# Kernel optimization log

Measured on AMD Instinct MI355X. Metric: run time of the kernel, lower is better.

## Reference

```python
import jax, jax.numpy as jnp
import numpy as np
from jax import lax

PAD = 960          # tf.pad amount each side
LN_EPS = 1e-3      # keras LayerNormalization default epsilon


def _process(x, h, gamma, beta):
    """SmallConvNet: grouped 1D conv (per-channel learnable kernel) -> LayerNorm -> SiLU.
    x: (B, 2, 64), h: (2, 961) -> (B, 2, 1024). Dropout omitted (see notes)."""
    # grouped conv: each of the 2 'sequence' channels has its own length-961 kernel
    y = lax.conv_general_dilated(
        x, h[:, None, :],                 # kernel (O=2, I=1, W=961)
        window_strides=(1,), padding=[(PAD, PAD)],
        dimension_numbers=("NCH", "OIH", "NCH"),
        feature_group_count=2)            # (B, 2, 1024)
    mu = jnp.mean(y, axis=-1, keepdims=True)
    var = jnp.mean(jnp.square(y - mu), axis=-1, keepdims=True)
    ln = gamma * (y - mu) * lax.rsqrt(var + LN_EPS) + beta
    return jax.nn.silu(ln)


def reference(values, h, gamma, beta, symbols):
    # values: (B, 2, 64); symbols: (2, 64)
    vp = _process(values, h, gamma, beta)                              # (B, 2, 1024)
    sp = _process(jnp.zeros_like(values) + symbols, h, gamma, beta)    # (B, 2, 1024)
    # sign-based cosine-similarity attention: S[b,i,j] = mean_d sign(vp[b,j,d])*sign(vp[b,j,d]+sp[b,i,d])
    Xi = vp[:, None, :, :]   # (B, 1, N, D)
    Xj = sp[:, :, None, :]   # (B, N, 1, D)
    S = jnp.mean(jnp.sign(Xi) * jnp.sign(Xi + Xj), axis=-1)           # (B, N, N)
    scores = jax.nn.softmax(S, axis=-1)
    attn = jnp.einsum("bij,bjd->bid", scores, vp)                     # (B, N, D)
    return jax.nn.silu(attn * sp)


def setup_inputs() -> dict:
    key = jax.random.key(0)
    k1, k2, k3 = jax.random.split(key, 3)
    B, N, Din, D = 16384, 2, 64, 1024
    return {
        "values": jax.random.normal(k1, (B, N, Din), dtype=jnp.float32),
        "h": jax.random.normal(k2, (2, 961), dtype=jnp.float32),
        "gamma": jnp.ones((D,), dtype=jnp.float32),
        "beta": jnp.zeros((D,), dtype=jnp.float32),
        "symbols": jax.random.normal(k3, (N, Din), dtype=jnp.float32),
    }
```

## Files before the change

kernel.cpp:

```cpp
#include <hip/hip_runtime.h>

#define NB 4
#define LN_EPS 1e-3f

static __device__ __forceinline__ float sgnf(float x) {
    return (x > 0.f) ? 1.f : ((x < 0.f) ? -1.f : 0.f);
}
static __device__ __forceinline__ float siluf(float x) {
    return x / (1.f + __expf(-x));
}


__global__ __launch_bounds__(256) void hd_prep(
    const float* __restrict__ h, const float* __restrict__ symbols,
    const float* __restrict__ gamma, const float* __restrict__ beta,
    float* __restrict__ ws)
{
    __shared__ float h_pad[2][1088];
    __shared__ float x_s[2][64];
    __shared__ float red[4][2];
    const int t = threadIdx.x;

    for (int idx = t; idx < 2 * 1088; idx += 256) {
        const int c = idx / 1088, j = idx - c * 1088;
        float v = 0.f;
        if (j >= 63 && j <= 1023) v = h[c * 961 + (j - 63)];
        h_pad[c][j] = v;
        const int src = 1086 - j;
        float vr = 0.f;
        if (src >= 63 && src <= 1023) vr = h[c * 961 + (src - 63)];
        ws[c * 1088 + j] = vr;
    }
    if (t < 128) x_s[t >> 6][t & 63] = symbols[t];
    __syncthreads();

    const int c = t >> 7, tt = t & 127;
    const int lane = t & 63, wid = t >> 6;
    const int jbase = 1023 - tt;

    float acc[8];
    #pragma unroll
    for (int k = 0; k < 8; ++k) acc[k] = 0.f;

    #pragma unroll 8
    for (int i = 0; i < 64; ++i) {
        const float xv = x_s[c][i];
        #pragma unroll
        for (int k = 0; k < 8; ++k)
            acc[k] = fmaf(xv, h_pad[c][jbase + i - 128 * k], acc[k]);
    }

    float ps = 0.f, pq = 0.f;
    #pragma unroll
    for (int k = 0; k < 8; ++k) { ps += acc[k]; pq += acc[k] * acc[k]; }
    #pragma unroll
    for (int off = 32; off; off >>= 1) {
        ps += __shfl_xor(ps, off);
        pq += __shfl_xor(pq, off);
    }
    if (lane == 0) { red[wid][0] = ps; red[wid][1] = pq; }
    __syncthreads();

    const float sum = red[2 * c][0] + red[2 * c + 1][0];
    const float sq  = red[2 * c][1] + red[2 * c + 1][1];
    const float mu  = sum * (1.f / 1024.f);
    float var = sq * (1.f / 1024.f) - mu * mu;
    var = fmaxf(var, 0.f);
    const float rs = rsqrtf(var + LN_EPS);

    #pragma unroll
    for (int k = 0; k < 8; ++k) {
        const int d = tt + 128 * k;
        const float ln = (acc[k] - mu) * rs * gamma[d] + beta[d];
        ws[2176 + c * 1024 + d] = siluf(ln);
    }
}

__global__ __launch_bounds__(256, 4) void hd_main(
    const float* __restrict__ values,
    const float* __restrict__ gamma, const float* __restrict__ beta,
    const float* __restrict__ ws, float* __restrict__ out)
{
    __shared__ float hrev[2][1088];
    __shared__ float red[4][16];
    __shared__ float redf[16];
    __shared__ float red2[4][16];
    __shared__ float redf2[16];

    const int t = threadIdx.x;
    const int lane = t & 63, wid = t >> 6;
    const size_t b0 = (size_t)blockIdx.x * NB;

    for (int idx = t; idx < 2 * 1088; idx += 256)
        (&hrev[0][0])[idx] = ws[idx];
    __syncthreads();

    float acc[NB][2][4];
    #pragma unroll
    for (int b = 0; b < NB; ++b)
        #pragma unroll
        for (int c = 0; c < 2; ++c)
            #pragma unroll
            for (int k = 0; k < 4; ++k) acc[b][c][k] = 0.f;

    #pragma unroll 1
    for (int i0 = 0; i0 < 64; i0 += 8) {
        const int q0 = 56 + 4 * t - i0;
        float r[2][12];
        #pragma unroll
        for (int c = 0; c < 2; ++c) {
            const float4* p = reinterpret_cast<const float4*>(&hrev[c][q0]);
            const float4 a0 = p[0], a1 = p[1], a2 = p[2];
            r[c][0] = a0.x; r[c][1] = a0.y; r[c][2]  = a0.z; r[c][3]  = a0.w;
            r[c][4] = a1.x; r[c][5] = a1.y; r[c][6]  = a1.z; r[c][7]  = a1.w;
            r[c][8] = a2.x; r[c][9] = a2.y; r[c][10] = a2.z; r[c][11] = a2.w;
        }
        #pragma unroll
        for (int b = 0; b < NB; ++b) {
            #pragma unroll
            for (int c = 0; c < 2; ++c) {
                const float* xp = values + ((b0 + b) * 2 + c) * 64 + i0;
                #pragma unroll
                for (int il = 0; il < 8; ++il) {
                    const float xv = xp[il];
                    #pragma unroll
                    for (int k = 0; k < 4; ++k)
                        acc[b][c][k] = fmaf(xv, r[c][7 - il + k], acc[b][c][k]);
                }
            }
        }
    }

    {
        float v16[16];
        #pragma unroll
        for (int b = 0; b < NB; ++b)
            #pragma unroll
            for (int c = 0; c < 2; ++c) {
                const float a0 = acc[b][c][0], a1 = acc[b][c][1];
                const float a2 = acc[b][c][2], a3 = acc[b][c][3];
                v16[(b * 2 + c) * 2]     = a0 + a1 + a2 + a3;
                v16[(b * 2 + c) * 2 + 1] = a0 * a0 + a1 * a1 + a2 * a2 + a3 * a3;
            }
        #pragma unroll
        for (int off = 32; off; off >>= 1)
            #pragma unroll
            for (int v = 0; v < 16; ++v)
                v16[v] += __shfl_xor(v16[v], off);
        if (lane == 0) {
            #pragma unroll
            for (int v = 0; v < 16; ++v) red[wid][v] = v16[v];
        }
    }
    __syncthreads();
    if (t < 16) redf[t] = red[0][t] + red[1][t] + red[2][t] + red[3][t];
    __syncthreads();

    const float4 g4  = *reinterpret_cast<const float4*>(&gamma[4 * t]);
    const float4 be4 = *reinterpret_cast<const float4*>(&beta[4 * t]);
    float sp_r[2][4];
    #pragma unroll
    for (int a = 0; a < 2; ++a) {
        const float4 s4 = *reinterpret_cast<const float4*>(&ws[2176 + a * 1024 + 4 * t]);
        sp_r[a][0] = s4.x; sp_r[a][1] = s4.y; sp_r[a][2] = s4.z; sp_r[a][3] = s4.w;
    }
    const float gk[4] = {g4.x, g4.y, g4.z, g4.w};
    const float bk[4] = {be4.x, be4.y, be4.z, be4.w};

    #pragma unroll
    for (int b = 0; b < NB; ++b)
        #pragma unroll
        for (int c = 0; c < 2; ++c) {
            const float sum = redf[(b * 2 + c) * 2];
            const float sq  = redf[(b * 2 + c) * 2 + 1];
            const float mu  = sum * (1.f / 1024.f);
            float var = sq * (1.f / 1024.f) - mu * mu;
            var = fmaxf(var, 0.f);
            const float rs = rsqrtf(var + LN_EPS);
            #pragma unroll
            for (int k = 0; k < 4; ++k)
                acc[b][c][k] = siluf((acc[b][c][k] - mu) * rs * gk[k] + bk[k]);
        }

    {
        float v16[16];
        #pragma unroll
        for (int b = 0; b < NB; ++b)
            #pragma unroll
            for (int a = 0; a < 2; ++a)
                #pragma unroll
                for (int c = 0; c < 2; ++c) {
                    float s = 0.f;
                    #pragma unroll
                    for (int k = 0; k < 4; ++k)
                        s += sgnf(acc[b][c][k]) * sgnf(acc[b][c][k] + sp_r[a][k]);
                    v16[b * 4 + a * 2 + c] = s;
                }
        #pragma unroll
        for (int off = 32; off; off >>= 1)
            #pragma unroll
            for (int v = 0; v < 16; ++v)
                v16[v] += __shfl_xor(v16[v], off);
        if (lane == 0) {
            #pragma unroll
            for (int v = 0; v < 16; ++v) red2[wid][v] = v16[v];
        }
    }
    __syncthreads();
    if (t < 16) redf2[t] = red2[0][t] + red2[1][t] + red2[2][t] + red2[3][t];
    __syncthreads();

    #pragma unroll
    for (int b = 0; b < NB; ++b) {
        #pragma unroll
        for (int a = 0; a < 2; ++a) {
            const float s0 = redf2[b * 4 + a * 2 + 0] * (1.f / 1024.f);
            const float s1 = redf2[b * 4 + a * 2 + 1] * (1.f / 1024.f);
            const float m  = fmaxf(s0, s1);
            const float e0 = __expf(s0 - m), e1 = __expf(s1 - m);
            const float inv = 1.f / (e0 + e1);
            const float p0 = e0 * inv, p1 = e1 * inv;
            float4 o;
            o.x = siluf((p0 * acc[b][0][0] + p1 * acc[b][1][0]) * sp_r[a][0]);
            o.y = siluf((p0 * acc[b][0][1] + p1 * acc[b][1][1]) * sp_r[a][1]);
            o.z = siluf((p0 * acc[b][0][2] + p1 * acc[b][1][2]) * sp_r[a][2]);
            o.w = siluf((p0 * acc[b][0][3] + p1 * acc[b][1][3]) * sp_r[a][3]);
            *reinterpret_cast<float4*>(out + ((b0 + b) * 2 + a) * 1024 + 4 * t) = o;
        }
    }
}

extern "C" void kernel_launch(void* const* d_in, const int* in_sizes, int n_in,
                              void* d_out, int out_size, void* d_ws, size_t ws_size,
                              hipStream_t stream) {
    const float* values  = (const float*)d_in[0];
    const float* h       = (const float*)d_in[1];
    const float* gamma   = (const float*)d_in[2];
    const float* beta    = (const float*)d_in[3];
    const float* symbols = (const float*)d_in[4];
    float* out = (float*)d_out;
    float* ws  = (float*)d_ws;

    const int B = in_sizes[0] / 128;

    hipLaunchKernelGGL(hd_prep, dim3(1), dim3(256), 0, stream,
                       h, symbols, gamma, beta, ws);
    hipLaunchKernelGGL(hd_main, dim3(B / NB), dim3(256), 0, stream,
                       values, gamma, beta, ws, out);
}
```

Measured before the change: 131.3 us.

## Compute grouped conv with bf16x3 split MFMA using a prepacked Toeplitz B matrix

Recasts the per-channel 961-tap convolution as a matrix multiply on MFMA units. Each fp32 operand is split into three bf16 parts and recombined with eight 16x16x32 MFMAs to keep close to fp32 accuracy. A new prep kernel packs the Toeplitz filter matrix into MFMA lane layout in the workspace. The sign-product reduction is also replaced by integer sign-bit XOR counting. The path needs a larger workspace, falling back to the scalar kernel otherwise, and it adds an extra launch and per-tile B loads from global memory.

```diff
diff --git a/kernel.cpp b/kernel.cpp
--- a/kernel.cpp
+++ b/kernel.cpp
@@ -1,17 +1,333 @@
 #include <hip/hip_runtime.h>
 
-#define NB 4
 #define LN_EPS 1e-3f
+
+typedef __attribute__((ext_vector_type(8))) short bf16x8;
+typedef __attribute__((ext_vector_type(4))) float f32x4;
 
 static __device__ __forceinline__ float sgnf(float x) {
     return (x > 0.f) ? 1.f : ((x < 0.f) ? -1.f : 0.f);
 }
-static __device__ __forceinline__ float siluf(float x) {
-    return x / (1.f + __expf(-x));
-}
-
-
-__global__ __launch_bounds__(256) void hd_prep(
+static __device__ __forceinline__ float siluf(float x) { return x / (1.f + __expf(-x)); }
+
+static __device__ __forceinline__ unsigned short f2bf(float f) {
+    unsigned int u = __float_as_uint(f);
+    return (unsigned short)((u + 0x7fffu + ((u >> 16) & 1u)) >> 16);
+}
+static __device__ __forceinline__ float bf2f(unsigned short s) {
+    return __uint_as_float(((unsigned int)s) << 16);
+}
+static __device__ __forceinline__ void split3(float v, unsigned short& hi,
+                                              unsigned short& mid, unsigned short& lo) {
+    hi = f2bf(v);
+    const float r1 = v - bf2f(hi);
+    mid = f2bf(r1);
+    const float r2 = r1 - bf2f(mid);
+    lo = f2bf(r2);
+}
+
+#define SPOFF 196608
+
+__global__ __launch_bounds__(256) void hd_prep_sp(
+    const float* __restrict__ h, const float* __restrict__ symbols,
+    const float* __restrict__ gamma, const float* __restrict__ beta,
+    float* __restrict__ ws)
+{
+    __shared__ float h_pad[2][1088];
+    __shared__ float x_s[2][64];
+    __shared__ float red[4][2];
+    const int t = threadIdx.x;
+
+    for (int idx = t; idx < 2 * 1088; idx += 256) {
+        const int c = idx / 1088, j = idx - c * 1088;
+        float v = 0.f;
+        if (j >= 63 && j <= 1023) v = h[c * 961 + (j - 63)];
+        h_pad[c][j] = v;
+    }
+    if (t < 128) x_s[t >> 6][t & 63] = symbols[t];
+    __syncthreads();
+
+    const int c = t >> 7, tt = t & 127;
+    const int lane = t & 63, wid = t >> 6;
+    const int jbase = 1023 - tt;
+
+    float acc[8];
+    #pragma unroll
+    for (int k = 0; k < 8; ++k) acc[k] = 0.f;
+
+    #pragma unroll 8
+    for (int i = 0; i < 64; ++i) {
+        const float xv = x_s[c][i];
+        #pragma unroll
+        for (int k = 0; k < 8; ++k)
+            acc[k] = fmaf(xv, h_pad[c][jbase + i - 128 * k], acc[k]);
+    }
+
+    float ps = 0.f, pq = 0.f;
+    #pragma unroll
+    for (int k = 0; k < 8; ++k) { ps += acc[k]; pq += acc[k] * acc[k]; }
+    #pragma unroll
+    for (int off = 32; off; off >>= 1) {
+        ps += __shfl_xor(ps, off);
+        pq += __shfl_xor(pq, off);
+    }
+    if (lane == 0) { red[wid][0] = ps; red[wid][1] = pq; }
+    __syncthreads();
+
+    const float sum = red[2 * c][0] + red[2 * c + 1][0];
+    const float sq  = red[2 * c][1] + red[2 * c + 1][1];
+    const float mu  = sum * (1.f / 1024.f);
+    float var = sq * (1.f / 1024.f) - mu * mu;
+    var = fmaxf(var, 0.f);
+    const float rs = rsqrtf(var + LN_EPS);
+
+    #pragma unroll
+    for (int k = 0; k < 8; ++k) {
+        const int d = tt + 128 * k;
+        const float ln = (acc[k] - mu) * rs * gamma[d] + beta[d];
+        ws[SPOFF + c * 1024 + d] = siluf(ln);
+    }
+}
+
+__global__ __launch_bounds__(256) void hd_prep_bpack(
+    const float* __restrict__ h, float* __restrict__ ws)
+{
+    unsigned short* Bp = (unsigned short*)ws;
+    const int total = 2 * 2 * 64 * 64 * 8;
+    for (int e = blockIdx.x * 256 + threadIdx.x; e < total; e += gridDim.x * 256) {
+        const int j   = e & 7;
+        const int l   = (e >> 3) & 63;
+        const int ntg = (e >> 9) & 63;
+        const int ks  = (e >> 15) & 1;
+        const int c   = (e >> 16) & 1;
+        const int H = 1023 - (16 * ntg + (l & 15)) + 32 * ks + 8 * (l >> 4) + j;
+        float v = 0.f;
+        if (H >= 63 && H <= 1023) v = h[c * 961 + (H - 63)];
+        unsigned short hi, mid, lo;
+        split3(v, hi, mid, lo);
+        const int base = ((((c * 2 + ks) * 64 + ntg) * 64 + l) * 3) * 8 + j;
+        Bp[base]      = hi;
+        Bp[base + 8]  = mid;
+        Bp[base + 16] = lo;
+    }
+}
+
+__global__ __launch_bounds__(256, 2) void hd_main_mfma(
+    const float* __restrict__ values,
+    const float* __restrict__ gamma, const float* __restrict__ beta,
+    const float* __restrict__ ws, float* __restrict__ out)
+{
+    __shared__ float stats[4][4][2][4][2];
+    __shared__ int   sred [4][4][2][4][2];
+
+    const int t = threadIdx.x;
+    const int w = t >> 6, l = t & 63;
+    const int g = l >> 4, q = l & 15;
+    const int b0 = blockIdx.x * 16;
+
+    bf16x8 ahi[2][2], amd_[2][2], alo[2][2];
+    #pragma unroll
+    for (int c = 0; c < 2; ++c) {
+        #pragma unroll
+        for (int ks = 0; ks < 2; ++ks) {
+            const float* xp = values + ((size_t)(b0 + q) * 2 + c) * 64 + ks * 32 + g * 8;
+            const float4 x0 = *reinterpret_cast<const float4*>(xp);
+            const float4 x1 = *reinterpret_cast<const float4*>(xp + 4);
+            const float xv[8] = {x0.x, x0.y, x0.z, x0.w, x1.x, x1.y, x1.z, x1.w};
+            bf16x8 h8, m8, l8;
+            #pragma unroll
+            for (int j = 0; j < 8; ++j) {
+                unsigned short hb, mb, lb;
+                split3(xv[j], hb, mb, lb);
+                h8[j] = (short)hb;
+                m8[j] = (short)mb;
+                l8[j] = (short)lb;
+            }
+            ahi[c][ks] = h8;
+            amd_[c][ks] = m8;
+            alo[c][ks] = l8;
+        }
+    }
+
+    const bf16x8* Bv = reinterpret_cast<const bf16x8*>(ws) + (size_t)l * 3;
+    f32x4 acc[2][16];
+    #pragma unroll
+    for (int c = 0; c < 2; ++c)
+        #pragma unroll
+        for (int nt = 0; nt < 16; ++nt)
+            acc[c][nt] = (f32x4){0.f, 0.f, 0.f, 0.f};
+
+    #pragma unroll
+    for (int nt = 0; nt < 16; ++nt) {
+        const int ntg = w * 16 + nt;
+        #pragma unroll
+        for (int c = 0; c < 2; ++c) {
+            f32x4 ts = {0.f, 0.f, 0.f, 0.f};
+            f32x4 tm = {0.f, 0.f, 0.f, 0.f};
+            f32x4 th = {0.f, 0.f, 0.f, 0.f};
+            #pragma unroll
+            for (int ks = 0; ks < 2; ++ks) {
+                const bf16x8* p = Bv + (size_t)((c * 2 + ks) * 64 + ntg) * 192;
+                const bf16x8 bh = p[0], bm = p[1], bl = p[2];
+                ts = __builtin_amdgcn_mfma_f32_16x16x32_bf16(amd_[c][ks], bl, ts, 0, 0, 0);
+                ts = __builtin_amdgcn_mfma_f32_16x16x32_bf16(alo[c][ks], bm, ts, 0, 0, 0);
+                ts = __builtin_amdgcn_mfma_f32_16x16x32_bf16(ahi[c][ks], bl, ts, 0, 0, 0);
+                ts = __builtin_amdgcn_mfma_f32_16x16x32_bf16(amd_[c][ks], bm, ts, 0, 0, 0);
+                ts = __builtin_amdgcn_mfma_f32_16x16x32_bf16(alo[c][ks], bh, ts, 0, 0, 0);
+                tm = __builtin_amdgcn_mfma_f32_16x16x32_bf16(ahi[c][ks], bm, tm, 0, 0, 0);
+                tm = __builtin_amdgcn_mfma_f32_16x16x32_bf16(amd_[c][ks], bh, tm, 0, 0, 0);
+                th = __builtin_amdgcn_mfma_f32_16x16x32_bf16(ahi[c][ks], bh, th, 0, 0, 0);
+            }
+            #pragma unroll
+            for (int r = 0; r < 4; ++r)
+                acc[c][nt][r] = (ts[r] + tm[r]) + th[r];
+        }
+    }
+
+    {
+        float s_[2][4], q_[2][4];
+        #pragma unroll
+        for (int c = 0; c < 2; ++c)
+            #pragma unroll
+            for (int r = 0; r < 4; ++r) { s_[c][r] = 0.f; q_[c][r] = 0.f; }
+        #pragma unroll
+        for (int c = 0; c < 2; ++c)
+            #pragma unroll
+            for (int nt = 0; nt < 16; ++nt)
+                #pragma unroll
+                for (int r = 0; r < 4; ++r) {
+                    const float v = acc[c][nt][r];
+                    s_[c][r] += v;
+                    q_[c][r] += v * v;
+                }
+        #pragma unroll
+        for (int off = 1; off < 16; off <<= 1)
+            #pragma unroll
+            for (int c = 0; c < 2; ++c)
+                #pragma unroll
+                for (int r = 0; r < 4; ++r) {
+                    s_[c][r] += __shfl_xor(s_[c][r], off);
+                    q_[c][r] += __shfl_xor(q_[c][r], off);
+                }
+        if (q == 0) {
+            #pragma unroll
+            for (int c = 0; c < 2; ++c)
+                #pragma unroll
+                for (int r = 0; r < 4; ++r) {
+                    stats[w][g][c][r][0] = s_[c][r];
+                    stats[w][g][c][r][1] = q_[c][r];
+                }
+        }
+    }
+    __syncthreads();
+
+    float mu_[2][4], rs_[2][4];
+    #pragma unroll
+    for (int c = 0; c < 2; ++c)
+        #pragma unroll
+        for (int r = 0; r < 4; ++r) {
+            float S = 0.f, Q = 0.f;
+            #pragma unroll
+            for (int w2 = 0; w2 < 4; ++w2) {
+                S += stats[w2][g][c][r][0];
+                Q += stats[w2][g][c][r][1];
+            }
+            const float mu = S * (1.f / 1024.f);
+            float var = Q * (1.f / 1024.f) - mu * mu;
+            var = fmaxf(var, 0.f);
+            mu_[c][r] = mu;
+            rs_[c][r] = rsqrtf(var + LN_EPS);
+        }
+
+    const int dbase = w * 256 + q;
+    #pragma unroll
+    for (int nt = 0; nt < 16; ++nt) {
+        const int d = dbase + 16 * nt;
+        const float gam = gamma[d];
+        const float bet = beta[d];
+        #pragma unroll
+        for (int c = 0; c < 2; ++c)
+            #pragma unroll
+            for (int r = 0; r < 4; ++r)
+                acc[c][nt][r] = siluf((acc[c][nt][r] - mu_[c][r]) * rs_[c][r] * gam + bet);
+    }
+
+    int cnt[2][4][2];
+    #pragma unroll
+    for (int c = 0; c < 2; ++c)
+        #pragma unroll
+        for (int r = 0; r < 4; ++r) { cnt[c][r][0] = 0; cnt[c][r][1] = 0; }
+    #pragma unroll
+    for (int nt = 0; nt < 16; ++nt) {
+        const int d = dbase + 16 * nt;
+        const float sp0 = ws[SPOFF + d];
+        const float sp1 = ws[SPOFF + 1024 + d];
+        #pragma unroll
+        for (int c = 0; c < 2; ++c)
+            #pragma unroll
+            for (int r = 0; r < 4; ++r) {
+                const float v = acc[c][nt][r];
+                const unsigned int iv = __float_as_uint(v);
+                cnt[c][r][0] += (int)((iv ^ __float_as_uint(v + sp0)) >> 31);
+                cnt[c][r][1] += (int)((iv ^ __float_as_uint(v + sp1)) >> 31);
+            }
+    }
+    #pragma unroll
+    for (int off = 1; off < 16; off <<= 1)
+        #pragma unroll
+        for (int c = 0; c < 2; ++c)
+            #pragma unroll
+            for (int r = 0; r < 4; ++r) {
+                cnt[c][r][0] += __shfl_xor(cnt[c][r][0], off);
+                cnt[c][r][1] += __shfl_xor(cnt[c][r][1], off);
+            }
+    if (q == 0) {
+        #pragma unroll
+        for (int c = 0; c < 2; ++c)
+            #pragma unroll
+            for (int r = 0; r < 4; ++r) {
+                sred[w][g][c][r][0] = cnt[c][r][0];
+                sred[w][g][c][r][1] = cnt[c][r][1];
+            }
+    }
+    __syncthreads();
+
+    float p0_[4][2], p1_[4][2];
+    #pragma unroll
+    for (int r = 0; r < 4; ++r)
+        #pragma unroll
+        for (int a = 0; a < 2; ++a) {
+            int t0 = 0, t1 = 0;
+            #pragma unroll
+            for (int w2 = 0; w2 < 4; ++w2) {
+                t0 += sred[w2][g][0][r][a];
+                t1 += sred[w2][g][1][r][a];
+            }
+            const float S0 = 1.f - 2.f * (float)t0 * (1.f / 1024.f);
+            const float S1 = 1.f - 2.f * (float)t1 * (1.f / 1024.f);
+            const float m  = fmaxf(S0, S1);
+            const float e0 = __expf(S0 - m), e1 = __expf(S1 - m);
+            const float inv = 1.f / (e0 + e1);
+            p0_[r][a] = e0 * inv;
+            p1_[r][a] = e1 * inv;
+        }
+
+    #pragma unroll
+    for (int nt = 0; nt < 16; ++nt) {
+        const int d = dbase + 16 * nt;
+        const float sp01[2] = {ws[SPOFF + d], ws[SPOFF + 1024 + d]};
+        #pragma unroll
+        for (int r = 0; r < 4; ++r) {
+            #pragma unroll
+            for (int a = 0; a < 2; ++a) {
+                const float attn = p0_[r][a] * acc[0][nt][r] + p1_[r][a] * acc[1][nt][r];
+                out[((size_t)(b0 + 4 * g + r) * 2 + a) * 1024 + d] = siluf(attn * sp01[a]);
+            }
+        }
+    }
+}
+
+__global__ __launch_bounds__(256) void hd_prep_scalar(
     const float* __restrict__ h, const float* __restrict__ symbols,
     const float* __restrict__ gamma, const float* __restrict__ beta,
     float* __restrict__ ws)
@@ -76,7 +392,7 @@
     }
 }
 
-__global__ __launch_bounds__(256, 4) void hd_main(
+__global__ __launch_bounds__(256, 4) void hd_main_scalar(
     const float* __restrict__ values,
     const float* __restrict__ gamma, const float* __restrict__ beta,
     const float* __restrict__ ws, float* __restrict__ out)
@@ -89,15 +405,15 @@
 
     const int t = threadIdx.x;
     const int lane = t & 63, wid = t >> 6;
-    const size_t b0 = (size_t)blockIdx.x * NB;
+    const size_t b0 = (size_t)blockIdx.x * 4;
 
     for (int idx = t; idx < 2 * 1088; idx += 256)
         (&hrev[0][0])[idx] = ws[idx];
     __syncthreads();
 
-    float acc[NB][2][4];
-    #pragma unroll
-    for (int b = 0; b < NB; ++b)
+    float acc[4][2][4];
+    #pragma unroll
+    for (int b = 0; b < 4; ++b)
         #pragma unroll
         for (int c = 0; c < 2; ++c)
             #pragma unroll
@@ -116,7 +432,7 @@
             r[c][8] = a2.x; r[c][9] = a2.y; r[c][10] = a2.z; r[c][11] = a2.w;
         }
         #pragma unroll
-        for (int b = 0; b < NB; ++b) {
+        for (int b = 0; b < 4; ++b) {
             #pragma unroll
             for (int c = 0; c < 2; ++c) {
                 const float* xp = values + ((b0 + b) * 2 + c) * 64 + i0;
@@ -134,7 +450,7 @@
     {
         float v16[16];
         #pragma unroll
-        for (int b = 0; b < NB; ++b)
+        for (int b = 0; b < 4; ++b)
             #pragma unroll
             for (int c = 0; c < 2; ++c) {
                 const float a0 = acc[b][c][0], a1 = acc[b][c][1];
@@ -168,7 +484,7 @@
     const float bk[4] = {be4.x, be4.y, be4.z, be4.w};
 
     #pragma unroll
-    for (int b = 0; b < NB; ++b)
+    for (int b = 0; b < 4; ++b)
         #pragma unroll
         for (int c = 0; c < 2; ++c) {
             const float sum = redf[(b * 2 + c) * 2];
@@ -185,7 +501,7 @@
     {
         float v16[16];
         #pragma unroll
-        for (int b = 0; b < NB; ++b)
+        for (int b = 0; b < 4; ++b)
             #pragma unroll
             for (int a = 0; a < 2; ++a)
                 #pragma unroll
@@ -211,7 +527,7 @@
     __syncthreads();
 
     #pragma unroll
-    for (int b = 0; b < NB; ++b) {
+    for (int b = 0; b < 4; ++b) {
         #pragma unroll
         for (int a = 0; a < 2; ++a) {
             const float s0 = redf2[b * 4 + a * 2 + 0] * (1.f / 1024.f);
@@ -243,8 +559,16 @@
 
     const int B = in_sizes[0] / 128;
 
-    hipLaunchKernelGGL(hd_prep, dim3(1), dim3(256), 0, stream,
-                       h, symbols, gamma, beta, ws);
-    hipLaunchKernelGGL(hd_main, dim3(B / NB), dim3(256), 0, stream,
-                       values, gamma, beta, ws, out);
-}
+    if (ws_size >= 794624) {
+        hipLaunchKernelGGL(hd_prep_sp, dim3(1), dim3(256), 0, stream,
+                           h, symbols, gamma, beta, ws);
+        hipLaunchKernelGGL(hd_prep_bpack, dim3(256), dim3(256), 0, stream, h, ws);
+        hipLaunchKernelGGL(hd_main_mfma, dim3(B / 16), dim3(256), 0, stream,
+                           values, gamma, beta, ws, out);
+    } else {
+        hipLaunchKernelGGL(hd_prep_scalar, dim3(1), dim3(256), 0, stream,
+                           h, symbols, gamma, beta, ws);
+        hipLaunchKernelGGL(hd_main_scalar, dim3(B / 4), dim3(256), 0, stream,
+                           values, gamma, beta, ws, out);
+    }
+}
```

New measurement: 140.3 us. +6.8%, slower.
